# Kernel optimization log

Measured on AMD Instinct MI355X. Metric: run time of the kernel, lower is better.

## Reference

```python
import jax, jax.numpy as jnp
import numpy as np

B, N_NODES, E = 2, 4096, 16384
H, DQK, DV = 8, 16, 128
DV_HEAD = DV // H  # dim_v_head = dim_v // n_heads


def setup_inputs() -> dict:
    key = jax.random.key(0)
    k1, k2, k3, k4, k5 = jax.random.split(key, 5)
    return {
        "query_values": jax.random.normal(k1, (B, E, H * DQK), jnp.float32),
        "key_values": jax.random.normal(k2, (B, N_NODES, H * DQK), jnp.float32),
        "value_values": jax.random.normal(k3, (B, E, DV), jnp.float32),
        "query_indices": jax.random.randint(k4, (B, E, 2), 0, N_NODES, jnp.int32),
        "value_indices": jax.random.randint(k5, (B, E, 2), 0, N_NODES, jnp.int32),
    }


def _heads(x, d):
    # torch: stack(x.split(d, -1), 0)  => [N, H*d] -> [H, N, d], head-major chunks
    n = x.shape[0]
    return jnp.transpose(x.reshape(n, -1, d), (1, 0, 2))


def reference(query_values, key_values, value_values, query_indices, value_indices):
    b, eq, _ = query_values.shape
    n_nodes = key_values.shape[1]
    n = b * n_nodes                       # total nodes across batch
    nv = b * eq                           # total value/query edges (full mask)
    node_ofs = (jnp.arange(b, dtype=query_indices.dtype) * n_nodes)[:, None, None]

    # _concat_batch: masked flatten (mask all True) + per-head split
    q = _heads(query_values.reshape(nv, -1), DQK)       # [H, Nq, d]
    k = _heads(key_values.reshape(n, -1), DQK)          # [H, n,  d]
    v = _heads(value_values.reshape(nv, -1), DV_HEAD)   # [H, Nv, dv_head]

    # _partial_key_value_sum: gather keys at edge row index, outer product, scatter-add by col
    v_idx = (value_indices + node_ofs).reshape(nv, 2)
    row, col = v_idx[:, 0], v_idx[:, 1]
    k_g = k[:, row, :]                                  # [H, Nv, d]
    # cat(unbind(h),-1).flatten(1,2): layout (n, i*DV + h*DV_HEAD + j)
    kv = jnp.einsum('hni,hnj->nihj', k_g, v).reshape(nv, DQK * DV)
    kg_flat = jnp.transpose(k_g, (1, 0, 2)).reshape(nv, H * DQK)
    kv_k = jnp.concatenate([kv, kg_flat], axis=-1)      # [Nv, DQK*DV + H*DQK]
    kv_k = jax.ops.segment_sum(kv_k, col, num_segments=n)  # coo(...).coalesce().to_dense()

    # _partial_apply_graph_query with dim1=2: gather by query col index
    q_idx = (query_indices + node_ofs).reshape(nv, 2)[:, 1]
    g = kv_k[q_idx]                                     # [Nq, DQK*DV + H*DQK]
    kv_q = jnp.transpose(g[:, :DQK * DV].reshape(nv, DQK, H, DV_HEAD), (2, 0, 1, 3))  # [H,Nq,d,dvh]
    k_sum = jnp.transpose(g[:, DQK * DV:].reshape(nv, H, DQK), (1, 0, 2))             # [H,Nq,d]

    att = jnp.einsum('hni,hnij->hnj', q, kv_q)          # [H, Nq, dv_head]
    qk = jnp.einsum('hni,hni->hn', q, k_sum)[..., None]
    qk = jnp.where(qk == 0, jnp.asarray(1e-5, qk.dtype), qk)
    att = att / qk
    att = jnp.transpose(att, (1, 0, 2)).reshape(b, eq, DV)

    # zero self-loop query edges (ord_q == 2 path)
    loop_mask = (query_indices[..., 0] != query_indices[..., 1])[..., None]
    return jnp.where(loop_mask, att, jnp.zeros((), att.dtype))
```

## Files before the change

### kernel.cpp

```cpp
#include <hip/hip_runtime.h>

#define B_SZ     2
#define E_EDGES  16384
#define N_NODES  4096
#define NTOT     (B_SZ * N_NODES)
#define NV       (B_SZ * E_EDGES)
#define DVTOT    128
#define LOG2_E   14
#define CAP      32

__device__ __forceinline__ int padidx(int f) { return f + ((f >> 4) << 2); }

__global__ __launch_bounds__(256) void zero_counts(int* __restrict__ p) {
    int i = blockIdx.x * blockDim.x + threadIdx.x;
    ((int4*)p)[i] = make_int4(0, 0, 0, 0);
}

__global__ __launch_bounds__(256) void fill_all(
    const int* __restrict__ qidx,
    const int* __restrict__ vidx,
    int*  __restrict__ ecnt,
    int*  __restrict__ qcnt,
    int2* __restrict__ ebuf,
    int*  __restrict__ qbuf)
{
    int e = blockIdx.x * blockDim.x + threadIdx.x;
    if (e >= NV) return;
    int ofs = (e >> LOG2_E) * N_NODES;

    int2 vi = ((const int2*)vidx)[e];
    int row = vi.x + ofs;
    int col = vi.y + ofs;
    int p = atomicAdd(&ecnt[col], 1);
    if (p < CAP) ebuf[col * CAP + p] = make_int2(e, row);

    int2 qi = ((const int2*)qidx)[e];
    int g  = qi.y + ofs;
    int pq = atomicAdd(&qcnt[g], 1);
    if (pq < CAP) qbuf[g * CAP + pq] = e | ((qi.x == qi.y) ? 0x80000000 : 0);
}

__global__ __launch_bounds__(256) void attn_node(
    const float* __restrict__ qv,
    const float* __restrict__ keys,
    const float* __restrict__ vals,
    const int*   __restrict__ ecnt,
    const int2*  __restrict__ ebuf,
    const int*   __restrict__ qcnt,
    const int*   __restrict__ qbuf,
    float*       __restrict__ out)
{
    __shared__ float sk[4][4][160];
    __shared__ float sq[4][4][160];

    int wid  = threadIdx.x >> 6;
    int lane = threadIdx.x & 63;
    int g    = blockIdx.x * 4 + wid;

    int nq = qcnt[g];  if (nq > CAP) nq = CAP;
    if (nq == 0) return;
    int deg = ecnt[g]; if (deg > CAP) deg = CAP;

    int h20 = (lane >> 3) * 20;
    int f2  = 2 * lane;

    float kva[16], kvb[16], ks[16];
#pragma unroll
    for (int i = 0; i < 16; ++i) { kva[i] = 0.0f; kvb[i] = 0.0f; ks[i] = 0.0f; }

    const int2* eb = ebuf + (size_t)g * CAP;
    for (int base = 0; base < deg; base += 4) {
        int n = deg - base; if (n > 4) n = 4;
        int2 r[4]; float2 v[4];
#pragma unroll
        for (int c = 0; c < 4; ++c)
            if (c < n) r[c] = eb[base + c];
#pragma unroll
        for (int c = 0; c < 4; ++c)
            if (c < n) {
                float2 kk = *(const float2*)(keys + (size_t)r[c].y * DVTOT + f2);
                *(float2*)&sk[wid][c][padidx(f2)] = kk;
                v[c] = *(const float2*)(vals + (size_t)r[c].x * DVTOT + f2);
            }
        __builtin_amdgcn_wave_barrier();
#pragma unroll
        for (int c = 0; c < 4; ++c)
            if (c < n) {
                const float4* kp = (const float4*)&sk[wid][c][h20];
                float4 k0 = kp[0], k1 = kp[1], k2 = kp[2], k3 = kp[3];
                float kk[16] = {k0.x,k0.y,k0.z,k0.w, k1.x,k1.y,k1.z,k1.w,
                                k2.x,k2.y,k2.z,k2.w, k3.x,k3.y,k3.z,k3.w};
#pragma unroll
                for (int i = 0; i < 16; ++i) {
                    ks[i]  += kk[i];
                    kva[i] += kk[i] * v[c].x;
                    kvb[i] += kk[i] * v[c].y;
                }
            }
        __builtin_amdgcn_wave_barrier();
    }

    const int* ql = qbuf + (size_t)g * CAP;
    for (int base = 0; base < nq; base += 4) {
        int n = nq - base; if (n > 4) n = 4;
        int t[4];
#pragma unroll
        for (int c = 0; c < 4; ++c)
            if (c < n) t[c] = ql[base + c];
#pragma unroll
        for (int c = 0; c < 4; ++c)
            if (c < n) {
                float2 qq = *(const float2*)(qv + (size_t)(t[c] & 0x7FFFFFFF) * DVTOT + f2);
                *(float2*)&sq[wid][c][padidx(f2)] = qq;
            }
        __builtin_amdgcn_wave_barrier();
#pragma unroll
        for (int c = 0; c < 4; ++c)
            if (c < n) {
                const float4* qp = (const float4*)&sq[wid][c][h20];
                float4 q0 = qp[0], q1 = qp[1], q2 = qp[2], q3 = qp[3];
                float qq[16] = {q0.x,q0.y,q0.z,q0.w, q1.x,q1.y,q1.z,q1.w,
                                q2.x,q2.y,q2.z,q2.w, q3.x,q3.y,q3.z,q3.w};
                float sa = 0.0f, sb = 0.0f, w = 0.0f;
#pragma unroll
                for (int i = 0; i < 16; ++i) {
                    sa += qq[i] * kva[i];
                    sb += qq[i] * kvb[i];
                    w  += qq[i] * ks[i];
                }
                float den = (w == 0.0f) ? 1e-5f : w;
                float inv = 1.0f / den;
                float2 o;
                o.x = (t[c] < 0) ? 0.0f : sa * inv;
                o.y = (t[c] < 0) ? 0.0f : sb * inv;
                *(float2*)(out + (size_t)(t[c] & 0x7FFFFFFF) * DVTOT + f2) = o;
            }
        __builtin_amdgcn_wave_barrier();
    }
}

extern "C" void kernel_launch(void* const* d_in, const int* in_sizes, int n_in,
                              void* d_out, int out_size, void* d_ws, size_t ws_size,
                              hipStream_t stream) {
    const float* qv   = (const float*)d_in[0];
    const float* keys = (const float*)d_in[1];
    const float* vals = (const float*)d_in[2];
    const int*   qidx = (const int*)d_in[3];
    const int*   vidx = (const int*)d_in[4];
    float* out = (float*)d_out;

    char* ws = (char*)d_ws;
    int*  ecnt = (int*)ws;
    int*  qcnt = ecnt + NTOT;
    int2* ebuf = (int2*)(ws + 65536);
    int*  qbuf = (int*)(ws + 65536 + NTOT * CAP * 8);

    zero_counts<<<16, 256, 0, stream>>>(ecnt);
    fill_all<<<(NV + 255) / 256, 256, 0, stream>>>(qidx, vidx, ecnt, qcnt, ebuf, qbuf);
    attn_node<<<NTOT / 4, 256, 0, stream>>>(qv, keys, vals, ecnt, ebuf, qcnt, qbuf, out);
}
```

Before: 36.81 us.

## Replace per-node counts with zero-sentinel lists and prefetch first edge and query batch

The whole workspace, including the edge and query bucket lists, is now zeroed, and stored indices are offset by one. Zero then marks the end of a list, so the attention kernel no longer reads the count arrays. Each wave loads the first four edge and query entries together and issues their key, value and query gathers before accumulating. This removes the dependent count-then-list load chain at the start of each wave. The cost is a much larger memset of the bucket buffers and extra sentinel checks in the loops.

```diff
diff --git a/kernel.cpp b/kernel.cpp
--- a/kernel.cpp
+++ b/kernel.cpp
@@ -9,11 +9,13 @@
 #define LOG2_E   14
 #define CAP      32
 
+#define ZERO_INT4 200704
+
 __device__ __forceinline__ int padidx(int f) { return f + ((f >> 4) << 2); }
 
-__global__ __launch_bounds__(256) void zero_counts(int* __restrict__ p) {
+__global__ __launch_bounds__(256) void zero_ws(int4* __restrict__ p) {
     int i = blockIdx.x * blockDim.x + threadIdx.x;
-    ((int4*)p)[i] = make_int4(0, 0, 0, 0);
+    p[i] = make_int4(0, 0, 0, 0);
 }
 
 __global__ __launch_bounds__(256) void fill_all(
@@ -32,21 +34,54 @@
     int row = vi.x + ofs;
     int col = vi.y + ofs;
     int p = atomicAdd(&ecnt[col], 1);
-    if (p < CAP) ebuf[col * CAP + p] = make_int2(e, row);
+    if (p < CAP) ebuf[col * CAP + p] = make_int2(e + 1, row);
 
     int2 qi = ((const int2*)qidx)[e];
     int g  = qi.y + ofs;
     int pq = atomicAdd(&qcnt[g], 1);
-    if (pq < CAP) qbuf[g * CAP + pq] = e | ((qi.x == qi.y) ? 0x80000000 : 0);
-}
+    if (pq < CAP) qbuf[g * CAP + pq] = (e + 1) | ((qi.x == qi.y) ? 0x80000000 : 0);
+}
+
+#define KACC(C)                                                          \
+    {                                                                    \
+        const float4* kp = (const float4*)&sk[wid][C][h20];              \
+        float4 k0 = kp[0], k1 = kp[1], k2 = kp[2], k3 = kp[3];           \
+        float kk[16] = {k0.x,k0.y,k0.z,k0.w, k1.x,k1.y,k1.z,k1.w,        \
+                        k2.x,k2.y,k2.z,k2.w, k3.x,k3.y,k3.z,k3.w};       \
+        _Pragma("unroll")                                                \
+        for (int i = 0; i < 16; ++i) {                                   \
+            ks[i]  += kk[i];                                             \
+            kva[i] += kk[i] * vvv[C].x;                                  \
+            kvb[i] += kk[i] * vvv[C].y;                                  \
+        }                                                                \
+    }
+
+#define QOUT(C, TREG)                                                    \
+    {                                                                    \
+        const float4* qp = (const float4*)&sq[wid][C][h20];              \
+        float4 q0 = qp[0], q1 = qp[1], q2 = qp[2], q3 = qp[3];           \
+        float qq[16] = {q0.x,q0.y,q0.z,q0.w, q1.x,q1.y,q1.z,q1.w,        \
+                        q2.x,q2.y,q2.z,q2.w, q3.x,q3.y,q3.z,q3.w};       \
+        float sa = 0.0f, sb = 0.0f, w = 0.0f;                            \
+        _Pragma("unroll")                                                \
+        for (int i = 0; i < 16; ++i) {                                   \
+            sa += qq[i] * kva[i];                                        \
+            sb += qq[i] * kvb[i];                                        \
+            w  += qq[i] * ks[i];                                         \
+        }                                                                \
+        float den = (w == 0.0f) ? 1e-5f : w;                             \
+        float inv = 1.0f / den;                                          \
+        float2 o;                                                        \
+        o.x = ((TREG) < 0) ? 0.0f : sa * inv;                            \
+        o.y = ((TREG) < 0) ? 0.0f : sb * inv;                            \
+        *(float2*)(out + (size_t)(((TREG) & 0x7FFFFFFF) - 1) * DVTOT + f2) = o; \
+    }
 
 __global__ __launch_bounds__(256) void attn_node(
     const float* __restrict__ qv,
     const float* __restrict__ keys,
     const float* __restrict__ vals,
-    const int*   __restrict__ ecnt,
     const int2*  __restrict__ ebuf,
-    const int*   __restrict__ qcnt,
     const int*   __restrict__ qbuf,
     float*       __restrict__ out)
 {
@@ -55,87 +90,103 @@
 
     int wid  = threadIdx.x >> 6;
     int lane = threadIdx.x & 63;
-    int g    = blockIdx.x * 4 + wid;
-
-    int nq = qcnt[g];  if (nq > CAP) nq = CAP;
-    if (nq == 0) return;
-    int deg = ecnt[g]; if (deg > CAP) deg = CAP;
+    int g    = __builtin_amdgcn_readfirstlane(blockIdx.x * 4 + wid);
 
     int h20 = (lane >> 3) * 20;
     int f2  = 2 * lane;
+    int pf2 = padidx(f2);
+
+    const int2* eb = ebuf + (size_t)g * CAP;
+    const int*  qb = qbuf + (size_t)g * CAP;
+
+    int qt[4];
+#pragma unroll
+    for (int c = 0; c < 4; ++c) qt[c] = qb[c];
+    int2 er[4];
+#pragma unroll
+    for (int c = 0; c < 4; ++c) er[c] = eb[c];
+
+    int nq0 = qt[0] ? (qt[1] ? (qt[2] ? (qt[3] ? 4 : 3) : 2) : 1) : 0;
+    if (nq0 == 0) return;
+    int dg0 = er[0].x ? (er[1].x ? (er[2].x ? (er[3].x ? 4 : 3) : 2) : 1) : 0;
+
+    float2 kkv[4], vvv[4], qqv[4];
+#pragma unroll
+    for (int c = 0; c < 4; ++c)
+        if (c < dg0) {
+            kkv[c] = *(const float2*)(keys + (size_t)er[c].y * DVTOT + f2);
+            vvv[c] = *(const float2*)(vals + (size_t)(er[c].x - 1) * DVTOT + f2);
+        }
+#pragma unroll
+    for (int c = 0; c < 4; ++c)
+        if (c < nq0)
+            qqv[c] = *(const float2*)(qv + (size_t)((qt[c] & 0x7FFFFFFF) - 1) * DVTOT + f2);
+#pragma unroll
+    for (int c = 0; c < 4; ++c)
+        if (c < dg0) *(float2*)&sk[wid][c][pf2] = kkv[c];
+#pragma unroll
+    for (int c = 0; c < 4; ++c)
+        if (c < nq0) *(float2*)&sq[wid][c][pf2] = qqv[c];
+    __builtin_amdgcn_wave_barrier();
 
     float kva[16], kvb[16], ks[16];
 #pragma unroll
     for (int i = 0; i < 16; ++i) { kva[i] = 0.0f; kvb[i] = 0.0f; ks[i] = 0.0f; }
 
-    const int2* eb = ebuf + (size_t)g * CAP;
-    for (int base = 0; base < deg; base += 4) {
-        int n = deg - base; if (n > 4) n = 4;
-        int2 r[4]; float2 v[4];
-#pragma unroll
-        for (int c = 0; c < 4; ++c)
-            if (c < n) r[c] = eb[base + c];
-#pragma unroll
-        for (int c = 0; c < 4; ++c)
-            if (c < n) {
-                float2 kk = *(const float2*)(keys + (size_t)r[c].y * DVTOT + f2);
-                *(float2*)&sk[wid][c][padidx(f2)] = kk;
-                v[c] = *(const float2*)(vals + (size_t)r[c].x * DVTOT + f2);
-            }
-        __builtin_amdgcn_wave_barrier();
-#pragma unroll
-        for (int c = 0; c < 4; ++c)
-            if (c < n) {
-                const float4* kp = (const float4*)&sk[wid][c][h20];
-                float4 k0 = kp[0], k1 = kp[1], k2 = kp[2], k3 = kp[3];
-                float kk[16] = {k0.x,k0.y,k0.z,k0.w, k1.x,k1.y,k1.z,k1.w,
-                                k2.x,k2.y,k2.z,k2.w, k3.x,k3.y,k3.z,k3.w};
-#pragma unroll
-                for (int i = 0; i < 16; ++i) {
-                    ks[i]  += kk[i];
-                    kva[i] += kk[i] * v[c].x;
-                    kvb[i] += kk[i] * v[c].y;
+#pragma unroll
+    for (int c = 0; c < 4; ++c)
+        if (c < dg0) KACC(c);
+
+    if (dg0 == 4) {
+        for (int base = 4; base < CAP; base += 4) {
+            int2 r[4];
+#pragma unroll
+            for (int c = 0; c < 4; ++c) r[c] = eb[base + c];
+            int n = r[0].x ? (r[1].x ? (r[2].x ? (r[3].x ? 4 : 3) : 2) : 1) : 0;
+            if (n == 0) break;
+#pragma unroll
+            for (int c = 0; c < 4; ++c)
+                if (c < n) {
+                    kkv[c] = *(const float2*)(keys + (size_t)r[c].y * DVTOT + f2);
+                    vvv[c] = *(const float2*)(vals + (size_t)(r[c].x - 1) * DVTOT + f2);
                 }
-            }
-        __builtin_amdgcn_wave_barrier();
-    }
-
-    const int* ql = qbuf + (size_t)g * CAP;
-    for (int base = 0; base < nq; base += 4) {
-        int n = nq - base; if (n > 4) n = 4;
-        int t[4];
-#pragma unroll
-        for (int c = 0; c < 4; ++c)
-            if (c < n) t[c] = ql[base + c];
-#pragma unroll
-        for (int c = 0; c < 4; ++c)
-            if (c < n) {
-                float2 qq = *(const float2*)(qv + (size_t)(t[c] & 0x7FFFFFFF) * DVTOT + f2);
-                *(float2*)&sq[wid][c][padidx(f2)] = qq;
-            }
-        __builtin_amdgcn_wave_barrier();
-#pragma unroll
-        for (int c = 0; c < 4; ++c)
-            if (c < n) {
-                const float4* qp = (const float4*)&sq[wid][c][h20];
-                float4 q0 = qp[0], q1 = qp[1], q2 = qp[2], q3 = qp[3];
-                float qq[16] = {q0.x,q0.y,q0.z,q0.w, q1.x,q1.y,q1.z,q1.w,
-                                q2.x,q2.y,q2.z,q2.w, q3.x,q3.y,q3.z,q3.w};
-                float sa = 0.0f, sb = 0.0f, w = 0.0f;
-#pragma unroll
-                for (int i = 0; i < 16; ++i) {
-                    sa += qq[i] * kva[i];
-                    sb += qq[i] * kvb[i];
-                    w  += qq[i] * ks[i];
-                }
-                float den = (w == 0.0f) ? 1e-5f : w;
-                float inv = 1.0f / den;
-                float2 o;
-                o.x = (t[c] < 0) ? 0.0f : sa * inv;
-                o.y = (t[c] < 0) ? 0.0f : sb * inv;
-                *(float2*)(out + (size_t)(t[c] & 0x7FFFFFFF) * DVTOT + f2) = o;
-            }
-        __builtin_amdgcn_wave_barrier();
+            __builtin_amdgcn_wave_barrier();
+#pragma unroll
+            for (int c = 0; c < 4; ++c)
+                if (c < n) *(float2*)&sk[wid][c][pf2] = kkv[c];
+            __builtin_amdgcn_wave_barrier();
+#pragma unroll
+            for (int c = 0; c < 4; ++c)
+                if (c < n) KACC(c);
+            if (n < 4) break;
+        }
+    }
+
+#pragma unroll
+    for (int c = 0; c < 4; ++c)
+        if (c < nq0) QOUT(c, qt[c]);
+
+    if (nq0 == 4) {
+        for (int base = 4; base < CAP; base += 4) {
+            int t[4];
+#pragma unroll
+            for (int c = 0; c < 4; ++c) t[c] = qb[base + c];
+            int n = t[0] ? (t[1] ? (t[2] ? (t[3] ? 4 : 3) : 2) : 1) : 0;
+            if (n == 0) break;
+#pragma unroll
+            for (int c = 0; c < 4; ++c)
+                if (c < n)
+                    qqv[c] = *(const float2*)(qv + (size_t)((t[c] & 0x7FFFFFFF) - 1) * DVTOT + f2);
+            __builtin_amdgcn_wave_barrier();
+#pragma unroll
+            for (int c = 0; c < 4; ++c)
+                if (c < n) *(float2*)&sq[wid][c][pf2] = qqv[c];
+            __builtin_amdgcn_wave_barrier();
+#pragma unroll
+            for (int c = 0; c < 4; ++c)
+                if (c < n) QOUT(c, t[c]);
+            if (n < 4) break;
+        }
     }
 }
 
@@ -152,10 +203,10 @@
     char* ws = (char*)d_ws;
     int*  ecnt = (int*)ws;
     int*  qcnt = ecnt + NTOT;
-    int2* ebuf = (int2*)(ws + 65536);
-    int*  qbuf = (int*)(ws + 65536 + NTOT * CAP * 8);
-
-    zero_counts<<<16, 256, 0, stream>>>(ecnt);
+    int2* ebuf = (int2*)(qcnt + NTOT);
+    int*  qbuf = (int*)(ebuf + (size_t)NTOT * CAP);
+
+    zero_ws<<<ZERO_INT4 / 256, 256, 0, stream>>>((int4*)ws);
     fill_all<<<(NV + 255) / 256, 256, 0, stream>>>(qidx, vidx, ecnt, qcnt, ebuf, qbuf);
-    attn_node<<<NTOT / 4, 256, 0, stream>>>(qv, keys, vals, ecnt, ebuf, qcnt, qbuf, out);
-}
+    attn_node<<<NTOT / 4, 256, 0, stream>>>(qv, keys, vals, ebuf, qbuf, out);
+}
```

New measurement: 31.46 us. 14.5% less time.

## Process two nodes per wave and prefetch first edge and query chunks

Applied to the files above, without the earlier changes.

Each wavefront now handles two destination nodes instead of one, and the launch grid is halved. All index lists, the first four key/value rows and the first four query rows for both nodes are loaded up front, so the memory latency of both nodes overlaps before any accumulation begins. The launch bounds gain an occupancy hint, and the workspace layout is packed contiguously. The cost is more registers and shared memory per wave and fewer waves in flight overall, which could cut the ability to hide latency.

```diff
diff --git a/kernel.cpp b/kernel.cpp
--- a/kernel.cpp
+++ b/kernel.cpp
@@ -11,9 +11,9 @@
 
 __device__ __forceinline__ int padidx(int f) { return f + ((f >> 4) << 2); }
 
-__global__ __launch_bounds__(256) void zero_counts(int* __restrict__ p) {
+__global__ __launch_bounds__(256) void zero_counts(int4* __restrict__ p) {
     int i = blockIdx.x * blockDim.x + threadIdx.x;
-    ((int4*)p)[i] = make_int4(0, 0, 0, 0);
+    p[i] = make_int4(0, 0, 0, 0);
 }
 
 __global__ __launch_bounds__(256) void fill_all(
@@ -40,102 +40,185 @@
     if (pq < CAP) qbuf[g * CAP + pq] = e | ((qi.x == qi.y) ? 0x80000000 : 0);
 }
 
-__global__ __launch_bounds__(256) void attn_node(
+#define KACC(SLOT, C, V)                                                  \
+    { const float4* kp = (const float4*)&sk[wid][SLOT][C][h20];           \
+      float4 k0=kp[0],k1=kp[1],k2=kp[2],k3=kp[3];                         \
+      float kk[16]={k0.x,k0.y,k0.z,k0.w,k1.x,k1.y,k1.z,k1.w,              \
+                    k2.x,k2.y,k2.z,k2.w,k3.x,k3.y,k3.z,k3.w};             \
+      _Pragma("unroll") for (int i=0;i<16;++i){                           \
+          ks[i]+=kk[i]; kva[i]+=kk[i]*(V).x; kvb[i]+=kk[i]*(V).y; } }
+
+#define QOUT(SLOT, C, T)                                                  \
+    { const float4* qp = (const float4*)&sq[wid][SLOT][C][h20];           \
+      float4 q0=qp[0],q1=qp[1],q2=qp[2],q3=qp[3];                         \
+      float qq[16]={q0.x,q0.y,q0.z,q0.w,q1.x,q1.y,q1.z,q1.w,              \
+                    q2.x,q2.y,q2.z,q2.w,q3.x,q3.y,q3.z,q3.w};             \
+      float sa=0.f,sb=0.f,w=0.f;                                          \
+      _Pragma("unroll") for (int i=0;i<16;++i){                           \
+          sa+=qq[i]*kva[i]; sb+=qq[i]*kvb[i]; w+=qq[i]*ks[i]; }           \
+      float den=(w==0.f)?1e-5f:w; float inv=1.f/den;                      \
+      float2 o; o.x=((T)<0)?0.f:sa*inv; o.y=((T)<0)?0.f:sb*inv;           \
+      *(float2*)(out + (size_t)((T)&0x7FFFFFFF)*DVTOT + f2) = o; }
+
+__global__ __launch_bounds__(256, 4) void attn_node(
     const float* __restrict__ qv,
     const float* __restrict__ keys,
     const float* __restrict__ vals,
     const int*   __restrict__ ecnt,
+    const int*   __restrict__ qcnt,
     const int2*  __restrict__ ebuf,
-    const int*   __restrict__ qcnt,
     const int*   __restrict__ qbuf,
     float*       __restrict__ out)
 {
-    __shared__ float sk[4][4][160];
-    __shared__ float sq[4][4][160];
+    __shared__ float sk[4][2][4][160];
+    __shared__ float sq[4][2][4][160];
 
     int wid  = threadIdx.x >> 6;
     int lane = threadIdx.x & 63;
-    int g    = blockIdx.x * 4 + wid;
-
-    int nq = qcnt[g];  if (nq > CAP) nq = CAP;
-    if (nq == 0) return;
-    int deg = ecnt[g]; if (deg > CAP) deg = CAP;
+    int gA = __builtin_amdgcn_readfirstlane(blockIdx.x * 8 + wid * 2);
+    int gB = gA + 1;
 
     int h20 = (lane >> 3) * 20;
     int f2  = 2 * lane;
+    int pf2 = padidx(f2);
+
+    const int2* ebA = ebuf + (size_t)gA * CAP;
+    const int*  qbA = qbuf + (size_t)gA * CAP;
+    const int2* ebB = ebuf + (size_t)gB * CAP;
+    const int*  qbB = qbuf + (size_t)gB * CAP;
+
+    int qcA = qcnt[gA], qcB = qcnt[gB];
+    int ecA = ecnt[gA], ecB = ecnt[gB];
+    int qtA[4], qtB[4]; int2 erA[4], erB[4];
+#pragma unroll
+    for (int c = 0; c < 4; ++c) {
+        qtA[c] = qbA[c]; qtB[c] = qbB[c];
+        erA[c] = ebA[c]; erB[c] = ebB[c];
+    }
+
+    int nqA = qcA < CAP ? qcA : CAP;
+    int nqB = qcB < CAP ? qcB : CAP;
+    if ((nqA | nqB) == 0) return;
+    int dgA = nqA ? (ecA < CAP ? ecA : CAP) : 0;
+    int dgB = nqB ? (ecB < CAP ? ecB : CAP) : 0;
+    int dgA0 = dgA < 4 ? dgA : 4, dgB0 = dgB < 4 ? dgB : 4;
+    int nqA0 = nqA < 4 ? nqA : 4, nqB0 = nqB < 4 ? nqB : 4;
+
+    float2 vA[4], vB[4];
+#pragma unroll
+    for (int c = 0; c < 4; ++c)
+        if (c < dgA0) {
+            *(float2*)&sk[wid][0][c][pf2] =
+                *(const float2*)(keys + (size_t)erA[c].y * DVTOT + f2);
+            vA[c] = *(const float2*)(vals + (size_t)erA[c].x * DVTOT + f2);
+        }
+#pragma unroll
+    for (int c = 0; c < 4; ++c)
+        if (c < nqA0)
+            *(float2*)&sq[wid][0][c][pf2] =
+                *(const float2*)(qv + (size_t)(qtA[c] & 0x7FFFFFFF) * DVTOT + f2);
+#pragma unroll
+    for (int c = 0; c < 4; ++c)
+        if (c < dgB0) {
+            *(float2*)&sk[wid][1][c][pf2] =
+                *(const float2*)(keys + (size_t)erB[c].y * DVTOT + f2);
+            vB[c] = *(const float2*)(vals + (size_t)erB[c].x * DVTOT + f2);
+        }
+#pragma unroll
+    for (int c = 0; c < 4; ++c)
+        if (c < nqB0)
+            *(float2*)&sq[wid][1][c][pf2] =
+                *(const float2*)(qv + (size_t)(qtB[c] & 0x7FFFFFFF) * DVTOT + f2);
+    __builtin_amdgcn_wave_barrier();
 
     float kva[16], kvb[16], ks[16];
-#pragma unroll
-    for (int i = 0; i < 16; ++i) { kva[i] = 0.0f; kvb[i] = 0.0f; ks[i] = 0.0f; }
-
-    const int2* eb = ebuf + (size_t)g * CAP;
-    for (int base = 0; base < deg; base += 4) {
-        int n = deg - base; if (n > 4) n = 4;
-        int2 r[4]; float2 v[4];
-#pragma unroll
-        for (int c = 0; c < 4; ++c)
-            if (c < n) r[c] = eb[base + c];
-#pragma unroll
-        for (int c = 0; c < 4; ++c)
-            if (c < n) {
-                float2 kk = *(const float2*)(keys + (size_t)r[c].y * DVTOT + f2);
-                *(float2*)&sk[wid][c][padidx(f2)] = kk;
-                v[c] = *(const float2*)(vals + (size_t)r[c].x * DVTOT + f2);
-            }
-        __builtin_amdgcn_wave_barrier();
-#pragma unroll
-        for (int c = 0; c < 4; ++c)
-            if (c < n) {
-                const float4* kp = (const float4*)&sk[wid][c][h20];
-                float4 k0 = kp[0], k1 = kp[1], k2 = kp[2], k3 = kp[3];
-                float kk[16] = {k0.x,k0.y,k0.z,k0.w, k1.x,k1.y,k1.z,k1.w,
-                                k2.x,k2.y,k2.z,k2.w, k3.x,k3.y,k3.z,k3.w};
-#pragma unroll
-                for (int i = 0; i < 16; ++i) {
-                    ks[i]  += kk[i];
-                    kva[i] += kk[i] * v[c].x;
-                    kvb[i] += kk[i] * v[c].y;
-                }
-            }
-        __builtin_amdgcn_wave_barrier();
+
+    if (nqA) {
+#pragma unroll
+        for (int i = 0; i < 16; ++i) { kva[i]=0.f; kvb[i]=0.f; ks[i]=0.f; }
+#pragma unroll
+        for (int c = 0; c < 4; ++c) if (c < dgA0) KACC(0, c, vA[c]);
+        if (dgA > 4) {
+            for (int base = 4; base < dgA; base += 4) {
+                int n = dgA - base; if (n > 4) n = 4;
+                int2 r[4]; float2 vv[4];
+#pragma unroll
+                for (int c = 0; c < 4; ++c) if (c < n) r[c] = ebA[base + c];
+#pragma unroll
+                for (int c = 0; c < 4; ++c)
+                    if (c < n) vv[c] = *(const float2*)(vals + (size_t)r[c].x * DVTOT + f2);
+                __builtin_amdgcn_wave_barrier();
+#pragma unroll
+                for (int c = 0; c < 4; ++c)
+                    if (c < n) *(float2*)&sk[wid][0][c][pf2] =
+                        *(const float2*)(keys + (size_t)r[c].y * DVTOT + f2);
+                __builtin_amdgcn_wave_barrier();
+#pragma unroll
+                for (int c = 0; c < 4; ++c) if (c < n) KACC(0, c, vv[c]);
+            }
+        }
+#pragma unroll
+        for (int c = 0; c < 4; ++c) if (c < nqA0) QOUT(0, c, qtA[c]);
+        if (nqA > 4) {
+            for (int base = 4; base < nqA; base += 4) {
+                int n = nqA - base; if (n > 4) n = 4;
+                int t[4];
+#pragma unroll
+                for (int c = 0; c < 4; ++c) if (c < n) t[c] = qbA[base + c];
+                __builtin_amdgcn_wave_barrier();
+#pragma unroll
+                for (int c = 0; c < 4; ++c)
+                    if (c < n) *(float2*)&sq[wid][0][c][pf2] =
+                        *(const float2*)(qv + (size_t)(t[c] & 0x7FFFFFFF) * DVTOT + f2);
+                __builtin_amdgcn_wave_barrier();
+#pragma unroll
+                for (int c = 0; c < 4; ++c) if (c < n) QOUT(0, c, t[c]);
+            }
+        }
     }
 
-    const int* ql = qbuf + (size_t)g * CAP;
-    for (int base = 0; base < nq; base += 4) {
-        int n = nq - base; if (n > 4) n = 4;
-        int t[4];
-#pragma unroll
-        for (int c = 0; c < 4; ++c)
-            if (c < n) t[c] = ql[base + c];
-#pragma unroll
-        for (int c = 0; c < 4; ++c)
-            if (c < n) {
-                float2 qq = *(const float2*)(qv + (size_t)(t[c] & 0x7FFFFFFF) * DVTOT + f2);
-                *(float2*)&sq[wid][c][padidx(f2)] = qq;
-            }
-        __builtin_amdgcn_wave_barrier();
-#pragma unroll
-        for (int c = 0; c < 4; ++c)
-            if (c < n) {
-                const float4* qp = (const float4*)&sq[wid][c][h20];
-                float4 q0 = qp[0], q1 = qp[1], q2 = qp[2], q3 = qp[3];
-                float qq[16] = {q0.x,q0.y,q0.z,q0.w, q1.x,q1.y,q1.z,q1.w,
-                                q2.x,q2.y,q2.z,q2.w, q3.x,q3.y,q3.z,q3.w};
-                float sa = 0.0f, sb = 0.0f, w = 0.0f;
-#pragma unroll
-                for (int i = 0; i < 16; ++i) {
-                    sa += qq[i] * kva[i];
-                    sb += qq[i] * kvb[i];
-                    w  += qq[i] * ks[i];
-                }
-                float den = (w == 0.0f) ? 1e-5f : w;
-                float inv = 1.0f / den;
-                float2 o;
-                o.x = (t[c] < 0) ? 0.0f : sa * inv;
-                o.y = (t[c] < 0) ? 0.0f : sb * inv;
-                *(float2*)(out + (size_t)(t[c] & 0x7FFFFFFF) * DVTOT + f2) = o;
-            }
-        __builtin_amdgcn_wave_barrier();
+    if (nqB) {
+#pragma unroll
+        for (int i = 0; i < 16; ++i) { kva[i]=0.f; kvb[i]=0.f; ks[i]=0.f; }
+#pragma unroll
+        for (int c = 0; c < 4; ++c) if (c < dgB0) KACC(1, c, vB[c]);
+        if (dgB > 4) {
+            for (int base = 4; base < dgB; base += 4) {
+                int n = dgB - base; if (n > 4) n = 4;
+                int2 r[4]; float2 vv[4];
+#pragma unroll
+                for (int c = 0; c < 4; ++c) if (c < n) r[c] = ebB[base + c];
+#pragma unroll
+                for (int c = 0; c < 4; ++c)
+                    if (c < n) vv[c] = *(const float2*)(vals + (size_t)r[c].x * DVTOT + f2);
+                __builtin_amdgcn_wave_barrier();
+#pragma unroll
+                for (int c = 0; c < 4; ++c)
+                    if (c < n) *(float2*)&sk[wid][1][c][pf2] =
+                        *(const float2*)(keys + (size_t)r[c].y * DVTOT + f2);
+                __builtin_amdgcn_wave_barrier();
+#pragma unroll
+                for (int c = 0; c < 4; ++c) if (c < n) KACC(1, c, vv[c]);
+            }
+        }
+#pragma unroll
+        for (int c = 0; c < 4; ++c) if (c < nqB0) QOUT(1, c, qtB[c]);
+        if (nqB > 4) {
+            for (int base = 4; base < nqB; base += 4) {
+                int n = nqB - base; if (n > 4) n = 4;
+                int t[4];
+#pragma unroll
+                for (int c = 0; c < 4; ++c) if (c < n) t[c] = qbB[base + c];
+                __builtin_amdgcn_wave_barrier();
+#pragma unroll
+                for (int c = 0; c < 4; ++c)
+                    if (c < n) *(float2*)&sq[wid][1][c][pf2] =
+                        *(const float2*)(qv + (size_t)(t[c] & 0x7FFFFFFF) * DVTOT + f2);
+                __builtin_amdgcn_wave_barrier();
+#pragma unroll
+                for (int c = 0; c < 4; ++c) if (c < n) QOUT(1, c, t[c]);
+            }
+        }
     }
 }
 
@@ -152,10 +235,10 @@
     char* ws = (char*)d_ws;
     int*  ecnt = (int*)ws;
     int*  qcnt = ecnt + NTOT;
-    int2* ebuf = (int2*)(ws + 65536);
-    int*  qbuf = (int*)(ws + 65536 + NTOT * CAP * 8);
-
-    zero_counts<<<16, 256, 0, stream>>>(ecnt);
+    int2* ebuf = (int2*)(qcnt + NTOT);
+    int*  qbuf = (int*)(ebuf + (size_t)NTOT * CAP);
+
+    zero_counts<<<16, 256, 0, stream>>>((int4*)ws);
     fill_all<<<(NV + 255) / 256, 256, 0, stream>>>(qidx, vidx, ecnt, qcnt, ebuf, qbuf);
-    attn_node<<<NTOT / 4, 256, 0, stream>>>(qv, keys, vals, ecnt, ebuf, qcnt, qbuf, out);
-}
+    attn_node<<<NTOT / 8, 256, 0, stream>>>(qv, keys, vals, ecnt, qcnt, ebuf, qbuf, out);
+}
```

Measured after the change: 37.07 us. No clear change (+0.7%).
